# Kernel tuning notes

Measured on AMD Instinct MI355X. Metric: run time of the kernel, lower is better.

Reference implementation:

```python
import jax, jax.numpy as jnp
from jax import lax
import numpy as np

ALPHA = 0.5   # weight of shape vs temporal component
GAMMA = 0.01  # soft-min temperature
BIG = 1e10    # finite stand-in for +inf borders (safe gradients)


def _softmin3(a, b, c, gamma):
    # -gamma * logsumexp(-x/gamma) over the three candidates
    z = jnp.stack([a, b, c], axis=0)
    return -gamma * jax.nn.logsumexp(-z / gamma, axis=0)


def _softdtw(D, gamma):
    """Soft-DTW value per problem. D: (B, N, N) cost matrix -> (B,).
    Classic DP: R[i,j] = D[i-1,j-1] + softmin(R[i-1,j-1], R[i-1,j], R[i,j-1])."""
    B, N, _ = D.shape
    # R row 0: R[0,0]=0, R[0,j>=1]=inf
    row0 = jnp.concatenate(
        [jnp.zeros((B, 1), D.dtype), jnp.full((B, N), BIG, D.dtype)], axis=1)
    left_init = jnp.full((B,), BIG, D.dtype)  # R[i,0] = inf for i>=1

    def row_step(R_prev, d_row):  # d_row: (B, N) = D[:, i-1, :]
        # per column j: diag = R_prev[j-1], up = R_prev[j], left = carry
        xs = (d_row.T, R_prev[:, :-1].T, R_prev[:, 1:].T)  # each (N, B)

        def col_step(r_left, x):
            d, r_diag, r_up = x
            r = d + _softmin3(r_diag, r_up, r_left, gamma)
            return r, r

        _, vals = lax.scan(col_step, left_init, xs)  # (N, B)
        R_row = jnp.concatenate([left_init[:, None], vals.T], axis=1)  # (B, N+1)
        return R_row, None

    R_last, _ = lax.scan(row_step, row0, jnp.transpose(D, (1, 0, 2)))
    return R_last[:, -1]  # R[N, N]


def _dilate(inp, tgt):
    B, C, N = inp.shape
    t = tgt.reshape(B * C, N)
    p = inp.reshape(B * C, N)
    # pairwise squared distances between 1-d points: D[k,i,j] = (t_i - p_j)^2
    D = (t[:, :, None] - p[:, None, :]) ** 2  # (B*C, N, N)

    # shape loss = soft-DTW value, averaged over channels
    sdtw = _softdtw(D, GAMMA)  # (B*C,)
    loss_shape = sdtw.reshape(B, C).mean(axis=1)  # (B,)

    # soft alignment path = gradient of soft-DTW w.r.t. the cost matrix
    E = jax.grad(lambda d: _softdtw(d, GAMMA).sum())(D)  # (B*C, N, N)

    # Omega[i,j] = (i - j)^2 temporal penalty
    idx = jnp.arange(1, N + 1, dtype=D.dtype)
    Omega = (idx[:, None] - idx[None, :]) ** 2  # (N, N)

    lt = jnp.sum(E * Omega, axis=(1, 2)) / (N * N)  # (B*C,)
    loss_temporal = lt.reshape(B, C).mean(axis=1)  # (B,)

    loss = (ALPHA * loss_shape + (1.0 - ALPHA) * loss_temporal).mean()
    return loss, loss_shape, loss_temporal


def setup_inputs() -> dict:
    key = jax.random.key(0)
    k1, k2 = jax.random.split(key)
    B, C, N = 64, 8, 160
    return {
        "input": jax.random.normal(k1, (B, C, N), jnp.float32),
        "target": jax.random.normal(k2, (B, C, N), jnp.float32),
    }


def reference(input, target):
    return _dilate(input, target)
```

## Files before the change

kernel.cpp:

```cpp
#include <hip/hip_runtime.h>
#include <math.h>


#define NN     160
#define BC_TOT 512
#define B_SZ   64
#define C_SZ   8
#define BIGC2  1e12f
#define SC2    12.01122405f
#define GLN2   0.0069314718056f
#define KPH    16
#define NCHUNK 20
#define NPHASE 22
#define RSZ    328

__device__ __forceinline__ float fexp2(float x) {
#if __has_builtin(__builtin_amdgcn_exp2f)
    return __builtin_amdgcn_exp2f(x);
#else
    return exp2f(x);
#endif
}
__device__ __forceinline__ float flog2(float x) {
#if __has_builtin(__builtin_amdgcn_logf)
    return __builtin_amdgcn_logf(x);
#else
    return log2f(x);
#endif
}
__device__ __forceinline__ float frcp(float x) {
#if __has_builtin(__builtin_amdgcn_rcpf)
    return __builtin_amdgcn_rcpf(x);
#else
    return 1.0f / x;
#endif
}
__device__ __forceinline__ float dpp_up1_inj(float old, float x) {
    int oi = __builtin_bit_cast(int, old);
    int xi = __builtin_bit_cast(int, x);
    return __builtin_bit_cast(float,
        __builtin_amdgcn_update_dpp(oi, xi, 0x138, 0xF, 0xF, false));
}
__device__ __forceinline__ void barrier_lds() {
    __asm__ __volatile__("" ::: "memory");
    __builtin_amdgcn_s_waitcnt(0xC07F);
    __builtin_amdgcn_s_barrier();
    __asm__ __volatile__("" ::: "memory");
}

__global__ __launch_bounds__(192)
void dtw_fwd_kernel(const float* __restrict__ input,
                    const float* __restrict__ target,
                    float* __restrict__ sdtw,
                    float* __restrict__ wlt)
{
    const int k    = blockIdx.x;
    const int tid  = threadIdx.x;
    const int w    = tid >> 6;
    const int lane = tid & 63;
    const bool rowok = (tid < NN);

    __shared__ __align__(16) float  Pp[4][520];
    __shared__ __align__(16) float2 bRG[2][RSZ];

    const float* tg = target + (size_t)k * NN;
    const float* pg = input  + (size_t)k * NN;
    for (int x = tid; x < 520; x += 192) {
        #pragma unroll
        for (int s = 0; s < 4; ++s) {
            const int v = x + s - 192;
            Pp[s][x] = ((unsigned)v < (unsigned)NN) ? pg[v] * SC2 : 0.0f;
        }
    }
    for (int x = tid; x < 2 * RSZ; x += 192) {
        float2 z; z.x = BIGC2; z.y = 0.0f;
        ((float2*)bRG)[x] = z;
    }
    const float trS = rowok ? tg[tid] * SC2 : 0.0f;
    barrier_lds();

    const bool isL0    = (lane == 0);
    const bool isL63p  = (lane == 63) && (w < 2);
    const bool useRing = (w > 0);
    const int  ti2     = 2 * (tid + 1);

    const int cLoF = 4 * w;
    const int cHiF = (4 * w + 13 < NCHUNK - 1) ? 4 * w + 13 : NCHUNK - 1;

    float r1c2 = BIGC2, u1c2 = BIGC2, u2c2 = BIGC2;
    float s1 = 0.0f, v1 = 0.0f, v2 = 0.0f;

    for (int t = 0; t < NPHASE; ++t) {
        const int c = t - w;
        if (c >= cLoF && c <= cHiF) {
            const int dlo = 2 + c * KPH;
            float rgx[18], rgd[18];
            if (useRing) {
                const float4* q = (const float4*)&bRG[w - 1][dlo - 2];
                #pragma unroll
                for (int x = 0; x < 9; ++x) {
                    const float4 v4 = q[x];
                    rgx[2 * x]     = v4.x; rgd[2 * x]     = v4.y;
                    rgx[2 * x + 1] = v4.z; rgd[2 * x + 1] = v4.w;
                }
            } else {
                #pragma unroll
                for (int x = 0; x < 18; ++x) { rgx[x] = BIGC2; rgd[x] = 0.0f; }
                if (c == 0) rgx[0] = 0.0f;
            }
            float pvvS[KPH];
            {
                const int A  = 192 - tid + KPH * c;
                const int sA = A & 3;
                const float4* pq = (const float4*)&Pp[sA][A - sA];
                #pragma unroll
                for (int x = 0; x < 4; ++x) {
                    const float4 p4 = pq[x];
                    pvvS[4 * x]     = p4.x; pvvS[4 * x + 1] = p4.y;
                    pvvS[4 * x + 2] = p4.z; pvvS[4 * x + 3] = p4.w;
                }
            }
            if (c == cLoF) {
                u1c2 = isL0 ? rgx[1] : BIGC2;
                u2c2 = isL0 ? rgx[0] : BIGC2;
                v1   = isL0 ? rgd[1] : 0.0f;
                v2   = isL0 ? rgd[0] : 0.0f;
            }
            float djf = (float)(dlo - ti2);
            #pragma unroll
            for (int u = 0; u < KPH; ++u) {
                const int d = dlo + u;
                const float vdC = u2c2;
                const float vuC = u1c2;
                const float vlC = r1c2;
                const float gd = v2, gu = v1, gl = s1;
                const float mnC = fminf(vdC, fminf(vuC, vlC));
                const float ed = fexp2(mnC - vdC);
                const float ev = fexp2(mnC - vuC);
                const float eh = fexp2(mnC - vlC);
                const float ss = ed + ev + eh;
                const float rs = frcp(ss);
                const float dtS = trS - pvvS[u];
                const float rC2 = __builtin_fmaf(dtS, dtS, mnC) - flog2(ss);
                const float num = __builtin_fmaf(ed, gd,
                                  __builtin_fmaf(ev, gu, eh * gl));
                const float rdot = __builtin_fmaf(num, rs, djf * djf);
                if (isL63p) {
                    float2 pub; pub.x = rC2; pub.y = rdot;
                    bRG[w][d] = pub;
                }
                if (d == 2 * NN) {
                    if (tid == NN - 1) {
                        sdtw[k] = rC2 * GLN2;
                        wlt[k]  = rdot * (1.0f / (NN * NN));
                    }
                }
                u2c2 = u1c2;
                u1c2 = dpp_up1_inj(rgx[u + 2], rC2);
                v2 = v1;
                v1 = dpp_up1_inj(rgd[u + 2], rdot);
                r1c2 = rC2;
                s1   = rdot;
                djf += 1.0f;
            }
        }
        barrier_lds();
    }
}

__global__ __launch_bounds__(64)
void finalize_kernel(const float* __restrict__ sdtw,
                     const float* __restrict__ wlt,
                     float* __restrict__ out)
{
    const int b = threadIdx.x;
    float ls = 0.0f, lt = 0.0f;
    #pragma unroll
    for (int c = 0; c < C_SZ; ++c) {
        ls += sdtw[b * C_SZ + c];
        lt += wlt[b * C_SZ + c];
    }
    ls *= (1.0f / C_SZ);
    lt *= (1.0f / C_SZ);
    out[1 + b]        = ls;
    out[1 + B_SZ + b] = lt;
    float v = 0.5f * ls + 0.5f * lt;
    #pragma unroll
    for (int o = 32; o > 0; o >>= 1) v += __shfl_down(v, o);
    if (b == 0) out[0] = v * (1.0f / B_SZ);
}

extern "C" void kernel_launch(void* const* d_in, const int* in_sizes, int n_in,
                              void* d_out, int out_size, void* d_ws, size_t ws_size,
                              hipStream_t stream) {
    const float* input  = (const float*)d_in[0];
    const float* target = (const float*)d_in[1];
    float* out = (float*)d_out;

    float* sdtw = (float*)d_ws;
    float* wlt  = sdtw + BC_TOT;

    dtw_fwd_kernel<<<BC_TOT, 192, 0, stream>>>(input, target, sdtw, wlt);
    finalize_kernel<<<1, 64, 0, stream>>>(sdtw, wlt, out);
}
```

Baseline: 95.14 us.

## Run each soft-DTW wavefront in a single wave with three rows per lane

Replaces the three-wave anti-diagonal pipeline, which used an LDS ring buffer and block barriers between phases, with a single 64-lane wave where each lane owns three consecutive DP rows. Values pass between lanes only through DPP shifts, so all barriers and LDS ring traffic go away. The cost is three times more serial per-lane work per diagonal and inactive-cell masking. The wave also runs all 20 chunks instead of skipping inactive phases, and the block count stays at 512 with one wave each, which lowers per-block parallelism.

```diff
diff --git a/kernel.cpp b/kernel.cpp
--- a/kernel.cpp
+++ b/kernel.cpp
@@ -11,8 +11,6 @@
 #define GLN2   0.0069314718056f
 #define KPH    16
 #define NCHUNK 20
-#define NPHASE 22
-#define RSZ    328
 
 __device__ __forceinline__ float fexp2(float x) {
 #if __has_builtin(__builtin_amdgcn_exp2f)
@@ -41,130 +39,101 @@
     return __builtin_bit_cast(float,
         __builtin_amdgcn_update_dpp(oi, xi, 0x138, 0xF, 0xF, false));
 }
-__device__ __forceinline__ void barrier_lds() {
-    __asm__ __volatile__("" ::: "memory");
-    __builtin_amdgcn_s_waitcnt(0xC07F);
-    __builtin_amdgcn_s_barrier();
-    __asm__ __volatile__("" ::: "memory");
-}
 
-__global__ __launch_bounds__(192)
+__global__ __launch_bounds__(64, 1)
 void dtw_fwd_kernel(const float* __restrict__ input,
                     const float* __restrict__ target,
                     float* __restrict__ sdtw,
                     float* __restrict__ wlt)
 {
     const int k    = blockIdx.x;
-    const int tid  = threadIdx.x;
-    const int w    = tid >> 6;
-    const int lane = tid & 63;
-    const bool rowok = (tid < NN);
+    const int lane = threadIdx.x;
 
-    __shared__ __align__(16) float  Pp[4][520];
-    __shared__ __align__(16) float2 bRG[2][RSZ];
+    __shared__ __align__(16) float Pp[4][520];
 
     const float* tg = target + (size_t)k * NN;
     const float* pg = input  + (size_t)k * NN;
-    for (int x = tid; x < 520; x += 192) {
+    for (int x = lane; x < 520; x += 64) {
         #pragma unroll
         for (int s = 0; s < 4; ++s) {
             const int v = x + s - 192;
             Pp[s][x] = ((unsigned)v < (unsigned)NN) ? pg[v] * SC2 : 0.0f;
         }
     }
-    for (int x = tid; x < 2 * RSZ; x += 192) {
-        float2 z; z.x = BIGC2; z.y = 0.0f;
-        ((float2*)bRG)[x] = z;
+    float tr[3];
+    #pragma unroll
+    for (int u = 0; u < 3; ++u) {
+        int idx = 3 * lane + u;
+        idx = (idx > NN - 1) ? NN - 1 : idx;
+        tr[u] = tg[idx] * SC2;
     }
-    const float trS = rowok ? tg[tid] * SC2 : 0.0f;
-    barrier_lds();
+    __syncthreads();
 
-    const bool isL0    = (lane == 0);
-    const bool isL63p  = (lane == 63) && (w < 2);
-    const bool useRing = (w > 0);
-    const int  ti2     = 2 * (tid + 1);
+    float p1[3], p2[3], g1[3], g2[3];
+    #pragma unroll
+    for (int s = 0; s < 3; ++s) { p1[s] = BIGC2; p2[s] = BIGC2; g1[s] = 0.f; g2[s] = 0.f; }
+    float b1  = BIGC2;
+    float b2  = (lane == 0) ? 0.0f : BIGC2;
+    float gb1 = 0.0f, gb2 = 0.0f;
+    const float bigR = BIGC2, zeroR = 0.0f;
 
-    const int cLoF = 4 * w;
-    const int cHiF = (4 * w + 13 < NCHUNK - 1) ? 4 * w + 13 : NCHUNK - 1;
+    float dj[3];
+    #pragma unroll
+    for (int s = 0; s < 3; ++s) dj[s] = (float)(-(6 * lane + 2 * s));
 
-    float r1c2 = BIGC2, u1c2 = BIGC2, u2c2 = BIGC2;
-    float s1 = 0.0f, v1 = 0.0f, v2 = 0.0f;
-
-    for (int t = 0; t < NPHASE; ++t) {
-        const int c = t - w;
-        if (c >= cLoF && c <= cHiF) {
-            const int dlo = 2 + c * KPH;
-            float rgx[18], rgd[18];
-            if (useRing) {
-                const float4* q = (const float4*)&bRG[w - 1][dlo - 2];
-                #pragma unroll
-                for (int x = 0; x < 9; ++x) {
-                    const float4 v4 = q[x];
-                    rgx[2 * x]     = v4.x; rgd[2 * x]     = v4.y;
-                    rgx[2 * x + 1] = v4.z; rgd[2 * x + 1] = v4.w;
-                }
-            } else {
-                #pragma unroll
-                for (int x = 0; x < 18; ++x) { rgx[x] = BIGC2; rgd[x] = 0.0f; }
-                if (c == 0) rgx[0] = 0.0f;
+    int dlo = 2;
+    for (int c = 0; c < NCHUNK; ++c, dlo += KPH) {
+        float pvv[20];
+        {
+            const int A0 = 192 + dlo - 3 * lane - 4;
+            const int sA = A0 & 3;
+            const float4* pq = (const float4*)&Pp[sA][A0 - sA];
+            #pragma unroll
+            for (int x = 0; x < 5; ++x) {
+                const float4 v4 = pq[x];
+                pvv[4 * x]     = v4.x; pvv[4 * x + 1] = v4.y;
+                pvv[4 * x + 2] = v4.z; pvv[4 * x + 3] = v4.w;
             }
-            float pvvS[KPH];
-            {
-                const int A  = 192 - tid + KPH * c;
-                const int sA = A & 3;
-                const float4* pq = (const float4*)&Pp[sA][A - sA];
-                #pragma unroll
-                for (int x = 0; x < 4; ++x) {
-                    const float4 p4 = pq[x];
-                    pvvS[4 * x]     = p4.x; pvvS[4 * x + 1] = p4.y;
-                    pvvS[4 * x + 2] = p4.z; pvvS[4 * x + 3] = p4.w;
-                }
-            }
-            if (c == cLoF) {
-                u1c2 = isL0 ? rgx[1] : BIGC2;
-                u2c2 = isL0 ? rgx[0] : BIGC2;
-                v1   = isL0 ? rgd[1] : 0.0f;
-                v2   = isL0 ? rgd[0] : 0.0f;
-            }
-            float djf = (float)(dlo - ti2);
+        }
+        #pragma unroll
+        for (int u = 0; u < KPH; ++u) {
+            const int d = dlo + u;
+            float cur[3], gcur[3];
             #pragma unroll
-            for (int u = 0; u < KPH; ++u) {
-                const int d = dlo + u;
-                const float vdC = u2c2;
-                const float vuC = u1c2;
-                const float vlC = r1c2;
-                const float gd = v2, gu = v1, gl = s1;
-                const float mnC = fminf(vdC, fminf(vuC, vlC));
-                const float ed = fexp2(mnC - vdC);
-                const float ev = fexp2(mnC - vuC);
-                const float eh = fexp2(mnC - vlC);
+            for (int s = 0; s < 3; ++s) {
+                const float a  = (s == 0) ? b2  : p2[s - 1];
+                const float bu = (s == 0) ? b1  : p1[s - 1];
+                const float cl = p1[s];
+                const float ga = (s == 0) ? gb2 : g2[s - 1];
+                const float gu = (s == 0) ? gb1 : g1[s - 1];
+                const float gl = g1[s];
+                const float mn = fminf(a, fminf(bu, cl));
+                const float ed = fexp2(mn - a);
+                const float ev = fexp2(mn - bu);
+                const float eh = fexp2(mn - cl);
                 const float ss = ed + ev + eh;
                 const float rs = frcp(ss);
-                const float dtS = trS - pvvS[u];
-                const float rC2 = __builtin_fmaf(dtS, dtS, mnC) - flog2(ss);
-                const float num = __builtin_fmaf(ed, gd,
+                const float dtS = tr[s] - pvv[u + 2 - s];
+                const float rC2 = __builtin_fmaf(dtS, dtS, mn) - flog2(ss);
+                const bool act = d >= (3 * lane + s + 2);
+                cur[s] = act ? rC2 : BIGC2;
+                const float num = __builtin_fmaf(ed, ga,
                                   __builtin_fmaf(ev, gu, eh * gl));
-                const float rdot = __builtin_fmaf(num, rs, djf * djf);
-                if (isL63p) {
-                    float2 pub; pub.x = rC2; pub.y = rdot;
-                    bRG[w][d] = pub;
-                }
-                if (d == 2 * NN) {
-                    if (tid == NN - 1) {
-                        sdtw[k] = rC2 * GLN2;
-                        wlt[k]  = rdot * (1.0f / (NN * NN));
-                    }
-                }
-                u2c2 = u1c2;
-                u1c2 = dpp_up1_inj(rgx[u + 2], rC2);
-                v2 = v1;
-                v1 = dpp_up1_inj(rgd[u + 2], rdot);
-                r1c2 = rC2;
-                s1   = rdot;
-                djf += 1.0f;
+                gcur[s] = __builtin_fmaf(num, rs, dj[s] * dj[s]);
+                dj[s] += 1.0f;
+            }
+            b2  = b1;  b1  = dpp_up1_inj(bigR,  cur[2]);
+            gb2 = gb1; gb1 = dpp_up1_inj(zeroR, gcur[2]);
+            #pragma unroll
+            for (int s = 0; s < 3; ++s) {
+                p2[s] = p1[s]; p1[s] = cur[s];
+                g2[s] = g1[s]; g1[s] = gcur[s];
             }
         }
-        barrier_lds();
+    }
+    if (lane == 53) {
+        sdtw[k] = p2[0] * GLN2;
+        wlt[k]  = g2[0] * (1.0f / (NN * NN));
     }
 }
 
@@ -200,6 +169,6 @@
     float* sdtw = (float*)d_ws;
     float* wlt  = sdtw + BC_TOT;
 
-    dtw_fwd_kernel<<<BC_TOT, 192, 0, stream>>>(input, target, sdtw, wlt);
+    dtw_fwd_kernel<<<BC_TOT, 64, 0, stream>>>(input, target, sdtw, wlt);
     finalize_kernel<<<1, 64, 0, stream>>>(sdtw, wlt, out);
 }
```

Result: slower. 106.8 us (+12.2%).
